# Kernel tuning notes

Hardware: AMD Instinct MI355X
Metric: run time of the kernel (lower is better)

Reference implementation:

```python
import jax, jax.numpy as jnp
import numpy as np

N, E = 50000, 600000
IN_DIM, HID, HYP = 384, 128, 256
NUM_LAYERS = 3
TAU = 0.5
ALPHA = 0.1
EPS = 1e-10


def setup_inputs() -> dict:
    keys = jax.random.split(jax.random.key(0), 10)
    x = jax.random.normal(keys[0], (N, IN_DIM), dtype=jnp.float32)
    edge_index = jax.random.randint(keys[1], (2, E), 0, N, dtype=jnp.int32)
    gumbel_u = jax.random.uniform(keys[2], (N, HYP), dtype=jnp.float32, minval=1e-6, maxval=1.0 - 1e-6)
    # parameters (xavier-ish scaling)
    w_feat = jax.random.normal(keys[3], (IN_DIM, HID), dtype=jnp.float32) * np.float32(1.0 / np.sqrt(IN_DIM))
    b_feat = jnp.zeros((HID,), jnp.float32)
    w_hyper = jax.random.normal(keys[4], (HID, HYP), dtype=jnp.float32) * np.float32(np.sqrt(2.0 / (HID + HYP)))
    w_vis = jax.random.normal(keys[5], (HID, HID), dtype=jnp.float32) * np.float32(1.0 / np.sqrt(HID))
    b_vis = jnp.zeros((HID,), jnp.float32)
    w_txt = jax.random.normal(keys[6], (HID, HID), dtype=jnp.float32) * np.float32(1.0 / np.sqrt(HID))
    b_txt = jnp.zeros((HID,), jnp.float32)
    return {"x": x, "edge_index": edge_index, "gumbel_u": gumbel_u,
            "w_feat": w_feat, "b_feat": b_feat, "w_hyper": w_hyper,
            "w_vis": w_vis, "b_vis": b_vis, "w_txt": w_txt, "b_txt": b_txt}


def reference(x, edge_index, gumbel_u, w_feat, b_feat, w_hyper, w_vis, b_vis, w_txt, b_txt):
    src, dst = edge_index[0], edge_index[1]
    # LGConv gcn_norm (no self loops): deg from in-edges, norm = d_src^-1/2 * d_dst^-1/2
    deg = jax.ops.segment_sum(jnp.ones((E,), x.dtype), dst, num_segments=N)
    dinv = jnp.where(deg > 0, jnp.where(deg > 0, deg, 1.0) ** -0.5, 0.0)
    ew = dinv[src] * dinv[dst]  # [E]

    x_emb = x @ w_feat + b_feat  # [N, HID] (dropout p=0 / eval: identity)

    # stacked LightGCN propagation, mean over (num_layers+1) layer outputs
    acc = x_emb
    cur = x_emb
    for _ in range(NUM_LAYERS):
        cur = jax.ops.segment_sum(cur[src] * ew[:, None], dst, num_segments=N)
        acc = acc + cur
    local = acc / jnp.asarray(NUM_LAYERS + 1, x.dtype)

    # HGNN: gumbel-softmax soft assignment + two dense matmuls
    logits = x_emb @ w_hyper  # [N, HYP]
    g = -jnp.log(-jnp.log(gumbel_u + EPS) + EPS)
    Hm = jax.nn.softmax((logits + g) / TAU, axis=1)  # [N, HYP]
    lat = Hm.T @ x_emb            # [HYP, HID]
    hyper_out = Hm @ lat          # [N, HID]

    # F.normalize(p=2, dim=1) with eps clamp 1e-12
    nrm = jnp.maximum(jnp.linalg.norm(hyper_out, axis=1, keepdims=True), 1e-12)
    final = local + ALPHA * (hyper_out / nrm)

    x_vision = jax.nn.relu(final @ w_vis + b_vis)
    x_text = jax.nn.relu(final @ w_txt + b_txt)
    return final, x_vision, x_text
```

## Files before the change

### kernel.cpp

```cpp
#include <hip/hip_runtime.h>
#include <math.h>

#define N_NODES 50000
#define E_EDGES 600000
#define IN_DIM  384
#define HID     128
#define HYP     256

#define SCAN_NB ((N_NODES + 255) / 256)

typedef __attribute__((ext_vector_type(8))) short bf16x8;
typedef __attribute__((ext_vector_type(4))) float f32x4;
typedef _Float16 f16x4 __attribute__((ext_vector_type(4)));

__device__ __forceinline__ unsigned short f2bf(float f) {
    unsigned u = __builtin_bit_cast(unsigned, f);
    u = (u + 0x7FFFu + ((u >> 16) & 1u)) >> 16;
    return (unsigned short)u;
}

__device__ __forceinline__ bf16x8 cvt8(float4 p, float4 q) {
    bf16x8 a;
    a[0] = (short)f2bf(p.x); a[1] = (short)f2bf(p.y);
    a[2] = (short)f2bf(p.z); a[3] = (short)f2bf(p.w);
    a[4] = (short)f2bf(q.x); a[5] = (short)f2bf(q.y);
    a[6] = (short)f2bf(q.z); a[7] = (short)f2bf(q.w);
    return a;
}


__global__ void k_deg(const int* __restrict__ dst, int* __restrict__ deg) {
    int i = blockIdx.x * blockDim.x + threadIdx.x;
    if (i < E_EDGES) atomicAdd(&deg[dst[i]], 1);
}

__global__ __launch_bounds__(256) void k_scan1(const int* __restrict__ deg, int* __restrict__ bsum) {
    __shared__ int sh[256];
    int tid = threadIdx.x;
    int i = blockIdx.x * 256 + tid;
    sh[tid] = (i < N_NODES) ? deg[i] : 0;
    __syncthreads();
#pragma unroll
    for (int off = 128; off > 0; off >>= 1) {
        if (tid < off) sh[tid] += sh[tid + off];
        __syncthreads();
    }
    if (tid == 0) bsum[blockIdx.x] = sh[0];
}

__global__ __launch_bounds__(256) void k_scan2(const int* __restrict__ bsum, int* __restrict__ bbase,
                                               int* __restrict__ row_start) {
    __shared__ int sh[256];
    int tid = threadIdx.x;
    int v = (tid < SCAN_NB) ? bsum[tid] : 0;
    sh[tid] = v;
    __syncthreads();
#pragma unroll
    for (int off = 1; off < 256; off <<= 1) {
        int t = (tid >= off) ? sh[tid - off] : 0;
        __syncthreads();
        sh[tid] += t;
        __syncthreads();
    }
    if (tid < SCAN_NB) bbase[tid] = sh[tid] - v;
    if (tid == 0) row_start[N_NODES] = E_EDGES;
}

__global__ __launch_bounds__(256) void k_scan3(const int* __restrict__ deg, const int* __restrict__ bbase,
                                               int* __restrict__ row_start, float* __restrict__ dinv) {
    __shared__ int sh[256];
    int tid = threadIdx.x;
    int i = blockIdx.x * 256 + tid;
    int d = (i < N_NODES) ? deg[i] : 0;
    sh[tid] = d;
    __syncthreads();
#pragma unroll
    for (int off = 1; off < 256; off <<= 1) {
        int t = (tid >= off) ? sh[tid - off] : 0;
        __syncthreads();
        sh[tid] += t;
        __syncthreads();
    }
    if (i < N_NODES) {
        row_start[i] = sh[tid] - d + bbase[blockIdx.x];
        dinv[i] = (d > 0) ? rsqrtf((float)d) : 0.0f;
    }
}

__global__ void k_fill(const int* __restrict__ src, const int* __restrict__ dst,
                       const int* __restrict__ row_start, int* __restrict__ cnt,
                       const float* __restrict__ dinv, int2* __restrict__ csr_sw) {
    int i = blockIdx.x * blockDim.x + threadIdx.x;
    if (i < E_EDGES) {
        int d = dst[i], s = src[i];
        int pos = row_start[d] + atomicAdd(&cnt[d], 1);
        csr_sw[pos] = make_int2(s, __float_as_int(dinv[s] * dinv[d]));
    }
}


__global__ __launch_bounds__(256) void k_cvt_all(const float* __restrict__ wf, const float* __restrict__ wh,
                                                 const float* __restrict__ wv, const float* __restrict__ wt,
                                                 unsigned short* __restrict__ wfT, unsigned short* __restrict__ whT,
                                                 unsigned short* __restrict__ wvT, unsigned short* __restrict__ wtT) {
    int i = blockIdx.x * 256 + threadIdx.x;
    if (i < 49152) {
        int r = i >> 7, c = i & 127;
        wfT[(size_t)c * IN_DIM + r] = f2bf(wf[i]);
    } else if (i < 49152 + 32768) {
        int j = i - 49152;
        int r = j >> 8, c = j & 255;
        whT[(size_t)c * HID + r] = f2bf(wh[j]);
    } else if (i < 49152 + 32768 + 16384) {
        int j = i - 81920;
        int r = j >> 7, c = j & 127;
        wvT[(size_t)c * HID + r] = f2bf(wv[j]);
    } else {
        int j = i - 98304;
        int r = j >> 7, c = j & 127;
        wtT[(size_t)c * HID + r] = f2bf(wt[j]);
    }
}


__global__ __launch_bounds__(128) void k_emb(const float* __restrict__ x, const unsigned short* __restrict__ wfT,
                                             const float* __restrict__ bf_, float* __restrict__ x_emb,
                                             _Float16* __restrict__ x_embh) {
    __shared__ float red[16 * HID];
    int tid = threadIdx.x;
    int wid = tid >> 6;
    int lane = tid & 63;
    int l16 = lane & 15, quad = lane >> 4;
    int m0 = blockIdx.x * 16;
    const float* xrow = x + (size_t)(m0 + l16) * IN_DIM + wid * 192 + quad * 8;
    float4 P[6], Q[6];
#pragma unroll
    for (int kt = 0; kt < 6; ++kt) {
        P[kt] = *reinterpret_cast<const float4*>(xrow + kt * 32);
        Q[kt] = *reinterpret_cast<const float4*>(xrow + kt * 32 + 4);
    }
    f32x4 acc[8];
#pragma unroll
    for (int nt = 0; nt < 8; ++nt) acc[nt] = (f32x4){0.f, 0.f, 0.f, 0.f};
#pragma unroll
    for (int kt = 0; kt < 6; ++kt) {
        bf16x8 a = cvt8(P[kt], Q[kt]);
#pragma unroll
        for (int nt = 0; nt < 8; ++nt) {
            bf16x8 b = *reinterpret_cast<const bf16x8*>(
                &wfT[(size_t)(nt * 16 + l16) * IN_DIM + wid * 192 + kt * 32 + quad * 8]);
            acc[nt] = __builtin_amdgcn_mfma_f32_16x16x32_bf16(a, b, acc[nt], 0, 0, 0);
        }
    }
    if (wid == 1) {
#pragma unroll
        for (int nt = 0; nt < 8; ++nt)
#pragma unroll
            for (int r = 0; r < 4; ++r)
                red[(quad * 4 + r) * HID + nt * 16 + l16] = acc[nt][r];
    }
    __syncthreads();
    if (wid == 0) {
#pragma unroll
        for (int nt = 0; nt < 8; ++nt) {
            int col = nt * 16 + l16;
            float bias = bf_[col];
#pragma unroll
            for (int r = 0; r < 4; ++r) {
                int lrow = quad * 4 + r;
                float v = acc[nt][r] + red[lrow * HID + col] + bias;
                size_t o = (size_t)(m0 + lrow) * HID + col;
                x_emb[o] = v;
                x_embh[o] = (_Float16)v;
            }
        }
    }
}


__device__ __forceinline__ void fma4h(float4& a, const f16x4 v, float s) {
    a.x = fmaf((float)v.x, s, a.x);
    a.y = fmaf((float)v.y, s, a.y);
    a.z = fmaf((float)v.z, s, a.z);
    a.w = fmaf((float)v.w, s, a.w);
}

template <int INIT, int LAST>
__global__ __launch_bounds__(256) void k_prop(const _Float16* __restrict__ curh, _Float16* __restrict__ nxth,
                                              const float* __restrict__ base, float* __restrict__ accb,
                                              const int* __restrict__ row_start,
                                              const int2* __restrict__ csr_sw) {
    int tid = threadIdx.x;
    int n = blockIdx.x * 8 + (tid >> 5);
    int c4 = (tid & 31) * 4;
    int s = row_start[n];
    int e = row_start[n + 1];
    float4 a[8];
#pragma unroll
    for (int k = 0; k < 8; ++k) a[k] = (float4){0.f, 0.f, 0.f, 0.f};
    for (int i = s; i < e; i += 8) {
        int2 pk[8];
        float wk[8];
#pragma unroll
        for (int k = 0; k < 8; ++k) {
            int j = i + k;
            pk[k] = csr_sw[(j < e) ? j : s];
            wk[k] = (j < e) ? __int_as_float(pk[k].y) : 0.0f;
        }
        f16x4 v[8];
#pragma unroll
        for (int k = 0; k < 8; ++k)
            v[k] = *reinterpret_cast<const f16x4*>(&curh[(size_t)pk[k].x * HID + c4]);
#pragma unroll
        for (int k = 0; k < 8; ++k) fma4h(a[k], v[k], wk[k]);
    }
    a[0].x += a[1].x; a[0].y += a[1].y; a[0].z += a[1].z; a[0].w += a[1].w;
    a[2].x += a[3].x; a[2].y += a[3].y; a[2].z += a[3].z; a[2].w += a[3].w;
    a[4].x += a[5].x; a[4].y += a[5].y; a[4].z += a[5].z; a[4].w += a[5].w;
    a[6].x += a[7].x; a[6].y += a[7].y; a[6].z += a[7].z; a[6].w += a[7].w;
    a[0].x += a[2].x; a[0].y += a[2].y; a[0].z += a[2].z; a[0].w += a[2].w;
    a[4].x += a[6].x; a[4].y += a[6].y; a[4].z += a[6].z; a[4].w += a[6].w;
    a[0].x += a[4].x; a[0].y += a[4].y; a[0].z += a[4].z; a[0].w += a[4].w;
    size_t o = (size_t)n * HID + c4;
    if (!LAST) {
        f16x4 oh;
        oh.x = (_Float16)a[0].x; oh.y = (_Float16)a[0].y;
        oh.z = (_Float16)a[0].z; oh.w = (_Float16)a[0].w;
        *reinterpret_cast<f16x4*>(&nxth[o]) = oh;
    }
    float4 ac = *reinterpret_cast<const float4*>(&base[o]);
    ac.x += a[0].x; ac.y += a[0].y; ac.z += a[0].z; ac.w += a[0].w;
    *reinterpret_cast<float4*>(&accb[o]) = ac;
}


__global__ __launch_bounds__(64) void k_soft(const float* __restrict__ x_emb, const unsigned short* __restrict__ whT,
                                             const float* __restrict__ gu, float* __restrict__ Hm) {
    int lane = threadIdx.x & 63;
    int l16 = lane & 15, quad = lane >> 4;
    int m0 = blockIdx.x * 16;
    const float* xrow = x_emb + (size_t)(m0 + l16) * HID + quad * 8;
    f32x4 acc[16];
#pragma unroll
    for (int nt = 0; nt < 16; ++nt) acc[nt] = (f32x4){0.f, 0.f, 0.f, 0.f};
#pragma unroll
    for (int kt = 0; kt < HID / 32; ++kt) {
        float4 p = *reinterpret_cast<const float4*>(xrow + kt * 32);
        float4 q = *reinterpret_cast<const float4*>(xrow + kt * 32 + 4);
        bf16x8 a = cvt8(p, q);
#pragma unroll
        for (int nt = 0; nt < 16; ++nt) {
            bf16x8 b = *reinterpret_cast<const bf16x8*>(&whT[(size_t)(nt * 16 + l16) * HID + kt * 32 + quad * 8]);
            acc[nt] = __builtin_amdgcn_mfma_f32_16x16x32_bf16(a, b, acc[nt], 0, 0, 0);
        }
    }
#pragma unroll
    for (int nt = 0; nt < 16; ++nt) {
        int col = nt * 16 + l16;
#pragma unroll
        for (int r = 0; r < 4; ++r) {
            int row = m0 + quad * 4 + r;
            float u = gu[(size_t)row * HYP + col];
            float g = -logf(-logf(u + 1e-10f) + 1e-10f);
            acc[nt][r] = (acc[nt][r] + g) * 2.0f;
        }
    }
    float mx[4] = {-3.4e38f, -3.4e38f, -3.4e38f, -3.4e38f};
#pragma unroll
    for (int nt = 0; nt < 16; ++nt)
#pragma unroll
        for (int r = 0; r < 4; ++r) mx[r] = fmaxf(mx[r], acc[nt][r]);
#pragma unroll
    for (int r = 0; r < 4; ++r) {
        mx[r] = fmaxf(mx[r], __shfl_xor(mx[r], 1));
        mx[r] = fmaxf(mx[r], __shfl_xor(mx[r], 2));
        mx[r] = fmaxf(mx[r], __shfl_xor(mx[r], 4));
        mx[r] = fmaxf(mx[r], __shfl_xor(mx[r], 8));
    }
    float sm[4] = {0.f, 0.f, 0.f, 0.f};
#pragma unroll
    for (int nt = 0; nt < 16; ++nt)
#pragma unroll
        for (int r = 0; r < 4; ++r) {
            float e = __expf(acc[nt][r] - mx[r]);
            acc[nt][r] = e;
            sm[r] += e;
        }
#pragma unroll
    for (int r = 0; r < 4; ++r) {
        sm[r] += __shfl_xor(sm[r], 1);
        sm[r] += __shfl_xor(sm[r], 2);
        sm[r] += __shfl_xor(sm[r], 4);
        sm[r] += __shfl_xor(sm[r], 8);
        sm[r] = 1.0f / sm[r];
    }
#pragma unroll
    for (int nt = 0; nt < 16; ++nt) {
        int col = nt * 16 + l16;
#pragma unroll
        for (int r = 0; r < 4; ++r)
            Hm[(size_t)(m0 + quad * 4 + r) * HYP + col] = acc[nt][r] * sm[r];
    }
}


#define LAT_KC 384

__global__ __launch_bounds__(256) void k_lat(const float* __restrict__ Hm, const float* __restrict__ x_emb,
                                             float* __restrict__ part) {
    int htile = blockIdx.x & 1;
    int kc = blockIdx.x >> 1;
    const int chunk = (N_NODES + LAT_KC - 1) / LAT_KC;
    int start = kc * chunk;
    int end = min(N_NODES, start + chunk);
    int nn = end - start;
    int tid = threadIdx.x;
    int lh = (tid & 15) * 8;
    int d = (tid >> 4) * 8;
    const float* __restrict__ hp = Hm + (size_t)start * HYP + htile * 128 + lh;
    const float* __restrict__ xp = x_emb + (size_t)start * HID + d;
    float acc[8][8];
#pragma unroll
    for (int i = 0; i < 8; ++i)
#pragma unroll
        for (int j = 0; j < 8; ++j) acc[i][j] = 0.f;
#pragma unroll 2
    for (int n = 0; n < nn; ++n) {
        float4 a0 = *reinterpret_cast<const float4*>(hp);
        float4 a1 = *reinterpret_cast<const float4*>(hp + 4);
        float4 b0 = *reinterpret_cast<const float4*>(xp);
        float4 b1 = *reinterpret_cast<const float4*>(xp + 4);
        float av[8] = {a0.x, a0.y, a0.z, a0.w, a1.x, a1.y, a1.z, a1.w};
        float bv[8] = {b0.x, b0.y, b0.z, b0.w, b1.x, b1.y, b1.z, b1.w};
#pragma unroll
        for (int i = 0; i < 8; ++i)
#pragma unroll
            for (int j = 0; j < 8; ++j) acc[i][j] = fmaf(av[i], bv[j], acc[i][j]);
        hp += HYP;
        xp += HID;
    }
    float* __restrict__ pp = part + (size_t)blockIdx.x * (128 * 128) + (size_t)lh * 128 + d;
#pragma unroll
    for (int i = 0; i < 8; ++i) {
        float4 v0 = {acc[i][0], acc[i][1], acc[i][2], acc[i][3]};
        float4 v1 = {acc[i][4], acc[i][5], acc[i][6], acc[i][7]};
        *reinterpret_cast<float4*>(pp + i * 128) = v0;
        *reinterpret_cast<float4*>(pp + i * 128 + 4) = v1;
    }
}


__global__ __launch_bounds__(256) void k_lat_red(const float* __restrict__ part, unsigned short* __restrict__ latT) {
    int idx = blockIdx.x * 256 + threadIdx.x;
    int d = idx & 127;
    int h = idx >> 7;
    int htile = h >> 7;
    int lh = h & 127;
    const float* __restrict__ p0 = part + (size_t)htile * (128 * 128) + (size_t)lh * 128 + d;
    const size_t kstride = (size_t)2 * 128 * 128;
    float s0 = 0.f, s1 = 0.f, s2 = 0.f, s3 = 0.f;
#pragma unroll 4
    for (int k = 0; k < LAT_KC; k += 4) {
        s0 += p0[(size_t)k * kstride];
        s1 += p0[(size_t)(k + 1) * kstride];
        s2 += p0[(size_t)(k + 2) * kstride];
        s3 += p0[(size_t)(k + 3) * kstride];
    }
    latT[(size_t)d * HYP + h] = f2bf((s0 + s1) + (s2 + s3));
}


__global__ __launch_bounds__(64) void k_tail(const float* __restrict__ Hm, const unsigned short* __restrict__ latT,
                                             const float* __restrict__ accb,
                                             const unsigned short* __restrict__ wvT, const float* __restrict__ bv,
                                             const unsigned short* __restrict__ wtT, const float* __restrict__ bt,
                                             float* __restrict__ out_final, float* __restrict__ out_vis,
                                             float* __restrict__ out_txt) {
    __shared__ unsigned short fl[16 * HID];
    int lane = threadIdx.x & 63;
    int l16 = lane & 15, quad = lane >> 4;
    int m0 = blockIdx.x * 16;
    const float* hrow = Hm + (size_t)(m0 + l16) * HYP + quad * 8;
    f32x4 acc[8];
#pragma unroll
    for (int nt = 0; nt < 8; ++nt) acc[nt] = (f32x4){0.f, 0.f, 0.f, 0.f};
#pragma unroll
    for (int kt = 0; kt < HYP / 32; ++kt) {
        float4 p = *reinterpret_cast<const float4*>(hrow + kt * 32);
        float4 q = *reinterpret_cast<const float4*>(hrow + kt * 32 + 4);
        bf16x8 a = cvt8(p, q);
#pragma unroll
        for (int nt = 0; nt < 8; ++nt) {
            bf16x8 b = *reinterpret_cast<const bf16x8*>(&latT[(size_t)(nt * 16 + l16) * HYP + kt * 32 + quad * 8]);
            acc[nt] = __builtin_amdgcn_mfma_f32_16x16x32_bf16(a, b, acc[nt], 0, 0, 0);
        }
    }
    float ss[4] = {0.f, 0.f, 0.f, 0.f};
#pragma unroll
    for (int nt = 0; nt < 8; ++nt)
#pragma unroll
        for (int r = 0; r < 4; ++r) ss[r] = fmaf(acc[nt][r], acc[nt][r], ss[r]);
#pragma unroll
    for (int r = 0; r < 4; ++r) {
        ss[r] += __shfl_xor(ss[r], 1);
        ss[r] += __shfl_xor(ss[r], 2);
        ss[r] += __shfl_xor(ss[r], 4);
        ss[r] += __shfl_xor(ss[r], 8);
        ss[r] = 1.0f / fmaxf(sqrtf(ss[r]), 1e-12f);
    }
#pragma unroll
    for (int nt = 0; nt < 8; ++nt) {
        int col = nt * 16 + l16;
#pragma unroll
        for (int r = 0; r < 4; ++r) {
            int lrow = quad * 4 + r;
            size_t o = (size_t)(m0 + lrow) * HID + col;
            float f = accb[o] * 0.25f + 0.1f * (acc[nt][r] * ss[r]);
            out_final[o] = f;
            fl[lrow * HID + col] = f2bf(f);
        }
    }
    __syncthreads();
    f32x4 av[8], at4[8];
#pragma unroll
    for (int nt = 0; nt < 8; ++nt) {
        av[nt] = (f32x4){0.f, 0.f, 0.f, 0.f};
        at4[nt] = (f32x4){0.f, 0.f, 0.f, 0.f};
    }
#pragma unroll
    for (int kt = 0; kt < HID / 32; ++kt) {
        bf16x8 a = *reinterpret_cast<const bf16x8*>(&fl[l16 * HID + kt * 32 + quad * 8]);
#pragma unroll
        for (int nt = 0; nt < 8; ++nt) {
            bf16x8 b1 = *reinterpret_cast<const bf16x8*>(&wvT[(size_t)(nt * 16 + l16) * HID + kt * 32 + quad * 8]);
            bf16x8 b2 = *reinterpret_cast<const bf16x8*>(&wtT[(size_t)(nt * 16 + l16) * HID + kt * 32 + quad * 8]);
            av[nt] = __builtin_amdgcn_mfma_f32_16x16x32_bf16(a, b1, av[nt], 0, 0, 0);
            at4[nt] = __builtin_amdgcn_mfma_f32_16x16x32_bf16(a, b2, at4[nt], 0, 0, 0);
        }
    }
#pragma unroll
    for (int nt = 0; nt < 8; ++nt) {
        int col = nt * 16 + l16;
        float b1 = bv[col], b2 = bt[col];
#pragma unroll
        for (int r = 0; r < 4; ++r) {
            size_t o = (size_t)(m0 + quad * 4 + r) * HID + col;
            out_vis[o] = fmaxf(av[nt][r] + b1, 0.0f);
            out_txt[o] = fmaxf(at4[nt][r] + b2, 0.0f);
        }
    }
}


extern "C" void kernel_launch(void* const* d_in, const int* in_sizes, int n_in,
                              void* d_out, int out_size, void* d_ws, size_t ws_size,
                              hipStream_t stream) {
    const float* x      = (const float*)d_in[0];
    const int*   ei     = (const int*)d_in[1];
    const float* gu     = (const float*)d_in[2];
    const float* w_feat = (const float*)d_in[3];
    const float* b_feat = (const float*)d_in[4];
    const float* w_hyp  = (const float*)d_in[5];
    const float* w_vis  = (const float*)d_in[6];
    const float* b_vis  = (const float*)d_in[7];
    const float* w_txt  = (const float*)d_in[8];
    const float* b_txt  = (const float*)d_in[9];
    float* out = (float*)d_out;

    const int* srcv = ei;
    const int* dstv = ei + E_EDGES;

    char* p = (char*)d_ws;
    int*   deg     = (int*)p;   p += (size_t)N_NODES * 4;
    int*   cnt     = (int*)p;   p += (size_t)N_NODES * 4;
    float* lat     = (float*)p; p += (size_t)HYP * HID * 4;
    int*   rs      = (int*)p;   p += (size_t)(N_NODES + 1) * 4;
    float* dinv    = (float*)p; p += (size_t)N_NODES * 4;
    int2*  csr_sw  = (int2*)p;  p += (size_t)E_EDGES * 8;
    float* x_emb   = (float*)p; p += (size_t)N_NODES * HID * 4;
    float* bufA    = (float*)p; p += (size_t)N_NODES * HID * 4;
    float* bufB    = (float*)p; p += (size_t)N_NODES * HID * 4;
    float* accb    = (float*)p; p += (size_t)N_NODES * HID * 4;
    float* Hm      = (float*)p; p += (size_t)N_NODES * HYP * 4;
    unsigned short* wfT  = (unsigned short*)p; p += (size_t)HID * IN_DIM * 2;
    unsigned short* whT  = (unsigned short*)p; p += (size_t)HYP * HID * 2;
    unsigned short* wvT  = (unsigned short*)p; p += (size_t)HID * HID * 2;
    unsigned short* wtT  = (unsigned short*)p; p += (size_t)HID * HID * 2;
    unsigned short* latT = (unsigned short*)p; p += (size_t)HID * HYP * 2;
    int*   bsum    = (int*)p;   p += (size_t)SCAN_NB * 4;
    int*   bbase   = (int*)p;   p += (size_t)SCAN_NB * 4;

    _Float16* bufAh  = (_Float16*)bufA;
    _Float16* bufBh  = (_Float16*)bufB;
    _Float16* x_embh = (_Float16*)((char*)bufB + (size_t)N_NODES * HID * 2);
    float* latPart = bufA;

    (void)hipMemsetAsync(d_ws, 0, (size_t)(2 * N_NODES + HYP * HID) * 4, stream);

    k_cvt_all<<<448, 256, 0, stream>>>(w_feat, w_hyp, w_vis, w_txt, wfT, whT, wvT, wtT);

    k_emb<<<N_NODES / 16, 128, 0, stream>>>(x, wfT, b_feat, x_emb, x_embh);

    k_deg<<<(E_EDGES + 255) / 256, 256, 0, stream>>>(dstv, deg);
    k_scan1<<<SCAN_NB, 256, 0, stream>>>(deg, bsum);
    k_scan2<<<1, 256, 0, stream>>>(bsum, bbase, rs);
    k_scan3<<<SCAN_NB, 256, 0, stream>>>(deg, bbase, rs, dinv);
    k_fill<<<(E_EDGES + 255) / 256, 256, 0, stream>>>(srcv, dstv, rs, cnt, dinv, csr_sw);

    k_prop<1, 0><<<N_NODES / 8, 256, 0, stream>>>(x_embh, bufAh, x_emb, accb, rs, csr_sw);
    k_prop<0, 0><<<N_NODES / 8, 256, 0, stream>>>(bufAh, bufBh, accb, accb, rs, csr_sw);
    k_prop<0, 1><<<N_NODES / 8, 256, 0, stream>>>(bufBh, bufAh, accb, accb, rs, csr_sw);
    k_soft<<<N_NODES / 16, 64, 0, stream>>>(x_emb, whT, gu, Hm);
    k_lat<<<2 * LAT_KC, 256, 0, stream>>>(Hm, x_emb, latPart);
    k_lat_red<<<(HYP * HID) / 256, 256, 0, stream>>>(latPart, latT);
    k_tail<<<N_NODES / 16, 64, 0, stream>>>(Hm, latT, accb, wvT, b_vis, wtT, b_txt,
                                            out, out + (size_t)N_NODES * HID, out + (size_t)2 * N_NODES * HID);
}
```

Baseline: 619.1 us.

## Store embeddings and soft assignments in fp16 and fuse degree count into embedding

Drops the fp32 copy of the embedding and keeps only the fp16 copy. The soft-assignment matrix is now stored in fp16, which halves its write and its reads in the latent and tail kernels. The first propagation step seeds its accumulator from the fp16 embedding instead of the fp32 one. The degree-count atomics now run as extra blocks of the embedding kernel, removing a launch. In exchange, the local branch and the HGNN inputs lose precision.

```diff
diff --git a/kernel.cpp b/kernel.cpp
--- a/kernel.cpp
+++ b/kernel.cpp
@@ -8,10 +8,13 @@
 #define HYP     256
 
 #define SCAN_NB ((N_NODES + 255) / 256)
+#define EMB_NB  (N_NODES / 16)
+#define DEG_NB  ((E_EDGES + 127) / 128)
 
 typedef __attribute__((ext_vector_type(8))) short bf16x8;
 typedef __attribute__((ext_vector_type(4))) float f32x4;
 typedef _Float16 f16x4 __attribute__((ext_vector_type(4)));
+typedef _Float16 f16x8 __attribute__((ext_vector_type(8)));
 
 __device__ __forceinline__ unsigned short f2bf(float f) {
     unsigned u = __builtin_bit_cast(unsigned, f);
@@ -28,11 +31,13 @@
     return a;
 }
 
-
-__global__ void k_deg(const int* __restrict__ dst, int* __restrict__ deg) {
-    int i = blockIdx.x * blockDim.x + threadIdx.x;
-    if (i < E_EDGES) atomicAdd(&deg[dst[i]], 1);
-}
+__device__ __forceinline__ bf16x8 cvt8h(f16x8 h) {
+    bf16x8 a;
+#pragma unroll
+    for (int i = 0; i < 8; ++i) a[i] = (short)f2bf((float)h[i]);
+    return a;
+}
+
 
 __global__ __launch_bounds__(256) void k_scan1(const int* __restrict__ deg, int* __restrict__ bsum) {
     __shared__ int sh[256];
@@ -123,15 +128,21 @@
 }
 
 
-__global__ __launch_bounds__(128) void k_emb(const float* __restrict__ x, const unsigned short* __restrict__ wfT,
-                                             const float* __restrict__ bf_, float* __restrict__ x_emb,
-                                             _Float16* __restrict__ x_embh) {
+__global__ __launch_bounds__(128) void k_embdeg(const float* __restrict__ x, const unsigned short* __restrict__ wfT,
+                                                const float* __restrict__ bf_, _Float16* __restrict__ x_embh,
+                                                const int* __restrict__ dst, int* __restrict__ deg) {
+    int b = blockIdx.x;
+    if (b >= EMB_NB) {
+        int i = (b - EMB_NB) * 128 + threadIdx.x;
+        if (i < E_EDGES) atomicAdd(&deg[dst[i]], 1);
+        return;
+    }
     __shared__ float red[16 * HID];
     int tid = threadIdx.x;
     int wid = tid >> 6;
     int lane = tid & 63;
     int l16 = lane & 15, quad = lane >> 4;
-    int m0 = blockIdx.x * 16;
+    int m0 = b * 16;
     const float* xrow = x + (size_t)(m0 + l16) * IN_DIM + wid * 192 + quad * 8;
     float4 P[6], Q[6];
 #pragma unroll
@@ -147,9 +158,9 @@
         bf16x8 a = cvt8(P[kt], Q[kt]);
 #pragma unroll
         for (int nt = 0; nt < 8; ++nt) {
-            bf16x8 b = *reinterpret_cast<const bf16x8*>(
+            bf16x8 bfr = *reinterpret_cast<const bf16x8*>(
                 &wfT[(size_t)(nt * 16 + l16) * IN_DIM + wid * 192 + kt * 32 + quad * 8]);
-            acc[nt] = __builtin_amdgcn_mfma_f32_16x16x32_bf16(a, b, acc[nt], 0, 0, 0);
+            acc[nt] = __builtin_amdgcn_mfma_f32_16x16x32_bf16(a, bfr, acc[nt], 0, 0, 0);
         }
     }
     if (wid == 1) {
@@ -169,9 +180,7 @@
             for (int r = 0; r < 4; ++r) {
                 int lrow = quad * 4 + r;
                 float v = acc[nt][r] + red[lrow * HID + col] + bias;
-                size_t o = (size_t)(m0 + lrow) * HID + col;
-                x_emb[o] = v;
-                x_embh[o] = (_Float16)v;
+                x_embh[(size_t)(m0 + lrow) * HID + col] = (_Float16)v;
             }
         }
     }
@@ -187,7 +196,7 @@
 
 template <int INIT, int LAST>
 __global__ __launch_bounds__(256) void k_prop(const _Float16* __restrict__ curh, _Float16* __restrict__ nxth,
-                                              const float* __restrict__ base, float* __restrict__ accb,
+                                              float* __restrict__ accb,
                                               const int* __restrict__ row_start,
                                               const int2* __restrict__ csr_sw) {
     int tid = threadIdx.x;
@@ -228,26 +237,32 @@
         oh.z = (_Float16)a[0].z; oh.w = (_Float16)a[0].w;
         *reinterpret_cast<f16x4*>(&nxth[o]) = oh;
     }
-    float4 ac = *reinterpret_cast<const float4*>(&base[o]);
+    float4 ac;
+    if (INIT) {
+        f16x4 bh = *reinterpret_cast<const f16x4*>(&curh[o]);
+        ac = make_float4((float)bh.x, (float)bh.y, (float)bh.z, (float)bh.w);
+    } else {
+        ac = *reinterpret_cast<const float4*>(&accb[o]);
+    }
     ac.x += a[0].x; ac.y += a[0].y; ac.z += a[0].z; ac.w += a[0].w;
     *reinterpret_cast<float4*>(&accb[o]) = ac;
 }
 
 
-__global__ __launch_bounds__(64) void k_soft(const float* __restrict__ x_emb, const unsigned short* __restrict__ whT,
-                                             const float* __restrict__ gu, float* __restrict__ Hm) {
+__global__ __launch_bounds__(64) void k_soft(const _Float16* __restrict__ x_embh,
+                                             const unsigned short* __restrict__ whT,
+                                             const float* __restrict__ gu, _Float16* __restrict__ Hmh) {
     int lane = threadIdx.x & 63;
     int l16 = lane & 15, quad = lane >> 4;
     int m0 = blockIdx.x * 16;
-    const float* xrow = x_emb + (size_t)(m0 + l16) * HID + quad * 8;
+    const _Float16* xrow = x_embh + (size_t)(m0 + l16) * HID + quad * 8;
     f32x4 acc[16];
 #pragma unroll
     for (int nt = 0; nt < 16; ++nt) acc[nt] = (f32x4){0.f, 0.f, 0.f, 0.f};
 #pragma unroll
     for (int kt = 0; kt < HID / 32; ++kt) {
-        float4 p = *reinterpret_cast<const float4*>(xrow + kt * 32);
-        float4 q = *reinterpret_cast<const float4*>(xrow + kt * 32 + 4);
-        bf16x8 a = cvt8(p, q);
+        f16x8 h = *reinterpret_cast<const f16x8*>(xrow + kt * 32);
+        bf16x8 a = cvt8h(h);
 #pragma unroll
         for (int nt = 0; nt < 16; ++nt) {
             bf16x8 b = *reinterpret_cast<const bf16x8*>(&whT[(size_t)(nt * 16 + l16) * HID + kt * 32 + quad * 8]);
@@ -299,14 +314,14 @@
         int col = nt * 16 + l16;
 #pragma unroll
         for (int r = 0; r < 4; ++r)
-            Hm[(size_t)(m0 + quad * 4 + r) * HYP + col] = acc[nt][r] * sm[r];
+            Hmh[(size_t)(m0 + quad * 4 + r) * HYP + col] = (_Float16)(acc[nt][r] * sm[r]);
     }
 }
 
 
 #define LAT_KC 384
 
-__global__ __launch_bounds__(256) void k_lat(const float* __restrict__ Hm, const float* __restrict__ x_emb,
+__global__ __launch_bounds__(256) void k_lat(const _Float16* __restrict__ Hmh, const _Float16* __restrict__ x_embh,
                                              float* __restrict__ part) {
     int htile = blockIdx.x & 1;
     int kc = blockIdx.x >> 1;
@@ -317,8 +332,8 @@
     int tid = threadIdx.x;
     int lh = (tid & 15) * 8;
     int d = (tid >> 4) * 8;
-    const float* __restrict__ hp = Hm + (size_t)start * HYP + htile * 128 + lh;
-    const float* __restrict__ xp = x_emb + (size_t)start * HID + d;
+    const _Float16* __restrict__ hp = Hmh + (size_t)start * HYP + htile * 128 + lh;
+    const _Float16* __restrict__ xp = x_embh + (size_t)start * HID + d;
     float acc[8][8];
 #pragma unroll
     for (int i = 0; i < 8; ++i)
@@ -326,12 +341,11 @@
         for (int j = 0; j < 8; ++j) acc[i][j] = 0.f;
 #pragma unroll 2
     for (int n = 0; n < nn; ++n) {
-        float4 a0 = *reinterpret_cast<const float4*>(hp);
-        float4 a1 = *reinterpret_cast<const float4*>(hp + 4);
-        float4 b0 = *reinterpret_cast<const float4*>(xp);
-        float4 b1 = *reinterpret_cast<const float4*>(xp + 4);
-        float av[8] = {a0.x, a0.y, a0.z, a0.w, a1.x, a1.y, a1.z, a1.w};
-        float bv[8] = {b0.x, b0.y, b0.z, b0.w, b1.x, b1.y, b1.z, b1.w};
+        f16x8 ah = *reinterpret_cast<const f16x8*>(hp);
+        f16x8 bh = *reinterpret_cast<const f16x8*>(xp);
+        float av[8], bv[8];
+#pragma unroll
+        for (int i = 0; i < 8; ++i) { av[i] = (float)ah[i]; bv[i] = (float)bh[i]; }
 #pragma unroll
         for (int i = 0; i < 8; ++i)
 #pragma unroll
@@ -370,7 +384,7 @@
 }
 
 
-__global__ __launch_bounds__(64) void k_tail(const float* __restrict__ Hm, const unsigned short* __restrict__ latT,
+__global__ __launch_bounds__(64) void k_tail(const _Float16* __restrict__ Hmh, const unsigned short* __restrict__ latT,
                                              const float* __restrict__ accb,
                                              const unsigned short* __restrict__ wvT, const float* __restrict__ bv,
                                              const unsigned short* __restrict__ wtT, const float* __restrict__ bt,
@@ -380,15 +394,14 @@
     int lane = threadIdx.x & 63;
     int l16 = lane & 15, quad = lane >> 4;
     int m0 = blockIdx.x * 16;
-    const float* hrow = Hm + (size_t)(m0 + l16) * HYP + quad * 8;
+    const _Float16* hrow = Hmh + (size_t)(m0 + l16) * HYP + quad * 8;
     f32x4 acc[8];
 #pragma unroll
     for (int nt = 0; nt < 8; ++nt) acc[nt] = (f32x4){0.f, 0.f, 0.f, 0.f};
 #pragma unroll
     for (int kt = 0; kt < HYP / 32; ++kt) {
-        float4 p = *reinterpret_cast<const float4*>(hrow + kt * 32);
-        float4 q = *reinterpret_cast<const float4*>(hrow + kt * 32 + 4);
-        bf16x8 a = cvt8(p, q);
+        f16x8 h = *reinterpret_cast<const f16x8*>(hrow + kt * 32);
+        bf16x8 a = cvt8h(h);
 #pragma unroll
         for (int nt = 0; nt < 8; ++nt) {
             bf16x8 b = *reinterpret_cast<const bf16x8*>(&latT[(size_t)(nt * 16 + l16) * HYP + kt * 32 + quad * 8]);
@@ -471,48 +484,50 @@
     const int* dstv = ei + E_EDGES;
 
     char* p = (char*)d_ws;
-    int*   deg     = (int*)p;   p += (size_t)N_NODES * 4;
-    int*   cnt     = (int*)p;   p += (size_t)N_NODES * 4;
-    float* lat     = (float*)p; p += (size_t)HYP * HID * 4;
-    int*   rs      = (int*)p;   p += (size_t)(N_NODES + 1) * 4;
-    float* dinv    = (float*)p; p += (size_t)N_NODES * 4;
-    int2*  csr_sw  = (int2*)p;  p += (size_t)E_EDGES * 8;
-    float* x_emb   = (float*)p; p += (size_t)N_NODES * HID * 4;
-    float* bufA    = (float*)p; p += (size_t)N_NODES * HID * 4;
-    float* bufB    = (float*)p; p += (size_t)N_NODES * HID * 4;
-    float* accb    = (float*)p; p += (size_t)N_NODES * HID * 4;
-    float* Hm      = (float*)p; p += (size_t)N_NODES * HYP * 4;
-    unsigned short* wfT  = (unsigned short*)p; p += (size_t)HID * IN_DIM * 2;
-    unsigned short* whT  = (unsigned short*)p; p += (size_t)HYP * HID * 2;
-    unsigned short* wvT  = (unsigned short*)p; p += (size_t)HID * HID * 2;
-    unsigned short* wtT  = (unsigned short*)p; p += (size_t)HID * HID * 2;
-    unsigned short* latT = (unsigned short*)p; p += (size_t)HID * HYP * 2;
-    int*   bsum    = (int*)p;   p += (size_t)SCAN_NB * 4;
-    int*   bbase   = (int*)p;   p += (size_t)SCAN_NB * 4;
-
-    _Float16* bufAh  = (_Float16*)bufA;
-    _Float16* bufBh  = (_Float16*)bufB;
-    _Float16* x_embh = (_Float16*)((char*)bufB + (size_t)N_NODES * HID * 2);
+    auto carve = [&p](size_t bytes) {
+        char* r = p;
+        p += (bytes + 63) & ~(size_t)63;
+        return r;
+    };
+    int*      deg     = (int*)carve((size_t)N_NODES * 4);
+    int*      cnt     = (int*)carve((size_t)N_NODES * 4);
+    int*      rs      = (int*)carve((size_t)(N_NODES + 1) * 4);
+    float*    dinv    = (float*)carve((size_t)N_NODES * 4);
+    int2*     csr_sw  = (int2*)carve((size_t)E_EDGES * 8);
+    _Float16* x_embh  = (_Float16*)carve((size_t)N_NODES * HID * 2);
+    float*    bufA    = (float*)carve((size_t)N_NODES * HID * 4);
+    float*    bufB    = (float*)carve((size_t)N_NODES * HID * 4);
+    float*    accb    = (float*)carve((size_t)N_NODES * HID * 4);
+    _Float16* Hmh     = (_Float16*)carve((size_t)N_NODES * HYP * 2);
+    unsigned short* wfT  = (unsigned short*)carve((size_t)HID * IN_DIM * 2);
+    unsigned short* whT  = (unsigned short*)carve((size_t)HYP * HID * 2);
+    unsigned short* wvT  = (unsigned short*)carve((size_t)HID * HID * 2);
+    unsigned short* wtT  = (unsigned short*)carve((size_t)HID * HID * 2);
+    unsigned short* latT = (unsigned short*)carve((size_t)HID * HYP * 2);
+    int*      bsum    = (int*)carve((size_t)SCAN_NB * 4);
+    int*      bbase   = (int*)carve((size_t)SCAN_NB * 4);
+
+    _Float16* bufAh = (_Float16*)bufA;
+    _Float16* bufBh = (_Float16*)bufB;
     float* latPart = bufA;
 
-    (void)hipMemsetAsync(d_ws, 0, (size_t)(2 * N_NODES + HYP * HID) * 4, stream);
+    (void)hipMemsetAsync(d_ws, 0, (size_t)2 * N_NODES * 4 + 128, stream);
 
     k_cvt_all<<<448, 256, 0, stream>>>(w_feat, w_hyp, w_vis, w_txt, wfT, whT, wvT, wtT);
 
-    k_emb<<<N_NODES / 16, 128, 0, stream>>>(x, wfT, b_feat, x_emb, x_embh);
-
-    k_deg<<<(E_EDGES + 255) / 256, 256, 0, stream>>>(dstv, deg);
+    k_embdeg<<<EMB_NB + DEG_NB, 128, 0, stream>>>(x, wfT, b_feat, x_embh, dstv, deg);
+
     k_scan1<<<SCAN_NB, 256, 0, stream>>>(deg, bsum);
     k_scan2<<<1, 256, 0, stream>>>(bsum, bbase, rs);
     k_scan3<<<SCAN_NB, 256, 0, stream>>>(deg, bbase, rs, dinv);
     k_fill<<<(E_EDGES + 255) / 256, 256, 0, stream>>>(srcv, dstv, rs, cnt, dinv, csr_sw);
 
-    k_prop<1, 0><<<N_NODES / 8, 256, 0, stream>>>(x_embh, bufAh, x_emb, accb, rs, csr_sw);
-    k_prop<0, 0><<<N_NODES / 8, 256, 0, stream>>>(bufAh, bufBh, accb, accb, rs, csr_sw);
-    k_prop<0, 1><<<N_NODES / 8, 256, 0, stream>>>(bufBh, bufAh, accb, accb, rs, csr_sw);
-    k_soft<<<N_NODES / 16, 64, 0, stream>>>(x_emb, whT, gu, Hm);
-    k_lat<<<2 * LAT_KC, 256, 0, stream>>>(Hm, x_emb, latPart);
+    k_prop<1, 0><<<N_NODES / 8, 256, 0, stream>>>(x_embh, bufAh, accb, rs, csr_sw);
+    k_prop<0, 0><<<N_NODES / 8, 256, 0, stream>>>(bufAh, bufBh, accb, rs, csr_sw);
+    k_prop<0, 1><<<N_NODES / 8, 256, 0, stream>>>(bufBh, bufAh, accb, rs, csr_sw);
+    k_soft<<<N_NODES / 16, 64, 0, stream>>>(x_embh, whT, gu, Hmh);
+    k_lat<<<2 * LAT_KC, 256, 0, stream>>>(Hmh, x_embh, latPart);
     k_lat_red<<<(HYP * HID) / 256, 256, 0, stream>>>(latPart, latT);
-    k_tail<<<N_NODES / 16, 64, 0, stream>>>(Hm, latT, accb, wvT, b_vis, wtT, b_txt,
+    k_tail<<<N_NODES / 16, 64, 0, stream>>>(Hmh, latT, accb, wvT, b_vis, wtT, b_txt,
                                             out, out + (size_t)N_NODES * HID, out + (size_t)2 * N_NODES * HID);
 }
```

After: 563.7 us. 9.0% less time.
